# Kernel optimization log

Hardware: AMD Instinct MI355X
Metric: run time of the kernel (lower is better)

## Reference

```python
import jax, jax.numpy as jnp
import numpy as np
from jax import lax

STRIDE = 4

def grid_sample_nearest(feat, grid):
    # feat: (B, C, H, W); grid: (B, Ho, Wo, 2) normalized to [-1, 1], align_corners=True,
    # mode='nearest', padding_mode='zeros' (matches torch.nn.functional.grid_sample).
    B, C, H, W = feat.shape
    gx = (grid[..., 0] + 1.0) * 0.5 * (W - 1)
    gy = (grid[..., 1] + 1.0) * 0.5 * (H - 1)
    ix = jnp.round(gx).astype(jnp.int32)  # round-half-to-even == std::nearbyint
    iy = jnp.round(gy).astype(jnp.int32)
    valid = (ix >= 0) & (ix < W) & (iy >= 0) & (iy < H)
    ixc = jnp.clip(ix, 0, W - 1)
    iyc = jnp.clip(iy, 0, H - 1)
    out = jax.vmap(lambda f, y, x: f[:, y, x])(feat, iyc, ixc)  # (B, C, Ho, Wo)
    return out * valid[:, None, :, :].astype(feat.dtype)

def unfold_s(x, s):
    # F.unfold(x, kernel=(s,s), stride=s): (n,c,h,w) -> (n, c*s*s, h//s * w//s)
    n, c, h, w = x.shape
    h4, w4 = h // s, w // s
    x = x.reshape(n, c, h4, s, w4, s).transpose(0, 1, 3, 5, 2, 4)  # (n,c,kh,kw,h4,w4)
    return x.reshape(n, c * s * s, h4 * w4)

def fold_s(x, s, c, h, w):
    # F.fold, kernel=(s,s), stride=s (non-overlapping): (n, c*s*s, h4*w4) -> (n,c,h,w)
    n = x.shape[0]
    h4, w4 = h // s, w // s
    x = x.reshape(n, c, s, s, h4, w4).transpose(0, 1, 4, 2, 5, 3)  # (n,c,h4,kh,w4,kw)
    return x.reshape(n, c, h, w)

def _normalize(x, axis):
    return x / jnp.maximum(jnp.linalg.norm(x, axis=axis, keepdims=True), 1e-12)

def ltam_forward(curr_feat, index_feat_set_s1, anchor_feat, sparse_feat_set_s1,
                 sparse_feat_set_s2, sparse_feat_set_s3, location_feat,
                 fusion_w, fusion_b):
    s = STRIDE
    n, c, h, w = anchor_feat.shape
    t = sparse_feat_set_s1.shape[1]
    h4, w4 = h // s, w // s
    feat_len = c * s * s
    feat_num = h4 * w4

    # build normalized nearest-sampling grid from location map
    gf = location_feat.reshape(n, t, 2, h4, w4).transpose(0, 1, 3, 4, 2)  # (n,t,h4,w4,2)
    gx = 2.0 * gf[..., 0] / max(w4 - 1, 1) - 1.0
    gy = 2.0 * gf[..., 1] / max(h4 - 1, 1) - 1.0
    grid = jnp.stack([gx, gy], axis=-1).reshape(n * t, h4, w4, 2)

    def warp(fs):
        return grid_sample_nearest(fs.reshape(n * t, feat_len, h4, w4), grid)

    out_s1 = warp(sparse_feat_set_s1)   # (n*t, feat_len, h4, w4)
    out_s2 = warp(sparse_feat_set_s2)
    out_s3 = warp(sparse_feat_set_s3)
    idx_s1 = warp(index_feat_set_s1)

    # current-frame patch tokens, L2-normalized
    cf = unfold_s(curr_feat, s).transpose(0, 2, 1)          # (n, feat_num, feat_len)
    cf = _normalize(cf, axis=2)

    # index tokens per frame, L2-normalized, correlate with current tokens
    idx_tok = idx_s1.reshape(n, t, feat_len, feat_num).transpose(0, 3, 1, 2)  # (n,feat_num,t,feat_len)
    idx_tok = _normalize(idx_tok, axis=3)
    matrix_index = jnp.einsum('nptf,npf->npt', idx_tok, cf)  # (n, feat_num, t)

    corr_soft = jnp.max(matrix_index, axis=2)                # (n, feat_num)
    corr_index = jnp.argmax(matrix_index, axis=2)            # (n, feat_num)

    corr_soft_map = fold_s(jnp.broadcast_to(corr_soft[:, None, :], (n, feat_len, feat_num)),
                           s, c, h, w)                       # (n, c, h, w)

    def gather_fold(o):
        o = o.reshape(n, t, feat_len, feat_num)
        idx = jnp.broadcast_to(corr_index[:, None, None, :], (n, 1, feat_len, feat_num))
        g = jnp.take_along_axis(o, idx, axis=1)[:, 0]        # (n, feat_len, feat_num)
        return fold_s(g, s, c, h, w)

    f1 = gather_fold(out_s1)
    f2 = gather_fold(out_s2)
    f3 = gather_fold(out_s3)

    out = jnp.concatenate([f1, f2, f3], axis=1)              # (n, 3c, h, w)
    out = lax.conv_general_dilated(out, fusion_w, (1, 1), ((1, 1), (1, 1)),
                                   dimension_numbers=('NCHW', 'OIHW', 'NCHW'))
    out = out + fusion_b[None, :, None, None]
    out = out * corr_soft_map + anchor_feat
    return out

def setup_inputs() -> dict:
    key = jax.random.key(0)
    ks = jax.random.split(key, 10)
    n, t, c, h, w, s = 1, 4, 128, 192, 192, STRIDE
    h4, w4 = h // s, w // s
    feat_len = c * s * s
    inp = {
        'curr_feat': jax.random.normal(ks[0], (n, c, h, w), jnp.float32),
        'index_feat_set_s1': jax.random.normal(ks[1], (n, t, feat_len, h4, w4), jnp.float32),
        'anchor_feat': jax.random.normal(ks[2], (n, c, h, w), jnp.float32),
        'sparse_feat_set_s1': jax.random.normal(ks[3], (n, t, feat_len, h4, w4), jnp.float32),
        'sparse_feat_set_s2': jax.random.normal(ks[4], (n, t, feat_len, h4, w4), jnp.float32),
        'sparse_feat_set_s3': jax.random.normal(ks[5], (n, t, feat_len, h4, w4), jnp.float32),
        # unnormalized pixel coordinates in [0, dim-1] (h4 == w4 here)
        'location_feat': jax.random.uniform(ks[6], (n, 2 * t, h4, w4), jnp.float32) * (w4 - 1),
        'fusion_w': jax.random.normal(ks[7], (c, 3 * c, 3, 3), jnp.float32) * 0.02,
        'fusion_b': jax.random.normal(ks[8], (c,), jnp.float32) * 0.02,
    }
    return inp

def reference(curr_feat, index_feat_set_s1, anchor_feat, sparse_feat_set_s1,
              sparse_feat_set_s2, sparse_feat_set_s3, location_feat,
              fusion_w, fusion_b):
    return ltam_forward(curr_feat, index_feat_set_s1, anchor_feat, sparse_feat_set_s1,
                        sparse_feat_set_s2, sparse_feat_set_s3, location_feat,
                        fusion_w, fusion_b)
```

## Files before the change

### kernel.cpp

```cpp
#include <hip/hip_runtime.h>
#include <hip/hip_bf16.h>
#include <math.h>

#define T_FRAMES 4
#define C 128
#define H 192
#define W 192
#define H4 48
#define W4 48
#define FEAT_LEN 2048
#define FEAT_NUM 2304
#define HW (H*W)
#define NCH 384
#define KTOT 3456
#define PPX 194

typedef __bf16 bf16x8 __attribute__((ext_vector_type(8)));
typedef float f32x4 __attribute__((ext_vector_type(4)));

__device__ __forceinline__ void sample_loc(const float* __restrict__ loc, int k, int p,
                                           int& iy, int& ix, int& valid) {
    float gfx = loc[(2*k+0)*FEAT_NUM + p];
    float gfy = loc[(2*k+1)*FEAT_NUM + p];
    float gx = 2.0f*gfx/47.0f - 1.0f;
    float gy = 2.0f*gfy/47.0f - 1.0f;
    float fx = (gx + 1.0f)*0.5f*47.0f;
    float fy = (gy + 1.0f)*0.5f*47.0f;
    int jx = (int)rintf(fx);
    int jy = (int)rintf(fy);
    valid = (jx >= 0 && jx < W4 && jy >= 0 && jy < H4) ? 1 : 0;
    ix = min(max(jx, 0), W4-1);
    iy = min(max(jy, 0), H4-1);
}

__global__ __launch_bounds__(256) void k_tr(const float* __restrict__ src,
                                            float* __restrict__ dst) {
    __shared__ float lds[64*65];
    int p0 = blockIdx.x*64, f0 = blockIdx.y*64, k = blockIdx.z;
    const float* s = src + (size_t)k*FEAT_LEN*FEAT_NUM;
    float* d = dst + (size_t)k*FEAT_NUM*FEAT_LEN;
    int tid = threadIdx.x;
    int pl = tid & 63, fb = tid >> 6;
#pragma unroll
    for (int i = 0; i < 16; ++i) {
        int fl = fb*16 + i;
        lds[fl*65 + pl] = s[(size_t)(f0+fl)*FEAT_NUM + p0 + pl];
    }
    __syncthreads();
    int f4 = (tid & 15)*4, pb = tid >> 4;
#pragma unroll
    for (int i = 0; i < 4; ++i) {
        int pl2 = pb + i*16;
        float4 v = { lds[(f4+0)*65 + pl2], lds[(f4+1)*65 + pl2],
                     lds[(f4+2)*65 + pl2], lds[(f4+3)*65 + pl2] };
        *(float4*)&d[(size_t)(p0+pl2)*FEAT_LEN + f0 + f4] = v;
    }
}

__global__ __launch_bounds__(256) void k_trs(const float* __restrict__ s1,
                                             const float* __restrict__ s2,
                                             const float* __restrict__ s3,
                                             ushort* __restrict__ spT) {
    __shared__ float lds[64*65];
    int p0 = blockIdx.x*64, f0 = blockIdx.y*64;
    int z = blockIdx.z;
    int set = z >> 2, k = z & 3;
    const float* src = (set == 0) ? s1 : ((set == 1) ? s2 : s3);
    const float* s = src + (size_t)k*FEAT_LEN*FEAT_NUM;
    int tid = threadIdx.x;
    int pl = tid & 63, fb = tid >> 6;
#pragma unroll
    for (int i = 0; i < 16; ++i) {
        int fl = fb*16 + i;
        lds[fl*65 + pl] = s[(size_t)(f0+fl)*FEAT_NUM + p0 + pl];
    }
    __syncthreads();
    int fo = (tid & 7)*8, pr = tid >> 3;
#pragma unroll
    for (int i = 0; i < 2; ++i) {
        int row = pr + i*32;
        ushort vv[8];
#pragma unroll
        for (int j = 0; j < 8; ++j) {
            __hip_bfloat16 b = __float2bfloat16(lds[(fo+j)*65 + row]);
            vv[j] = *(ushort*)&b;
        }
        uint4 pk;
        pk.x = (uint)vv[0] | ((uint)vv[1] << 16);
        pk.y = (uint)vv[2] | ((uint)vv[3] << 16);
        pk.z = (uint)vv[4] | ((uint)vv[5] << 16);
        pk.w = (uint)vv[6] | ((uint)vv[7] << 16);
        *(uint4*)(spT + ((size_t)z*FEAT_NUM + p0 + row)*FEAT_LEN + f0 + fo) = pk;
    }
}

__global__ __launch_bounds__(256) void k_gather2(const ushort* __restrict__ spT,
                                                 const float* __restrict__ loc,
                                                 const int* __restrict__ corr_index,
                                                 ushort* __restrict__ cat) {
    __shared__ ushort tok[3*FEAT_LEN];
    int p = blockIdx.x;
    int y4 = p / W4, x4 = p - y4*W4;
    int tid = threadIdx.x;
    int k = corr_index[p];
    int iy, ix, valid;
    sample_loc(loc, k, p, iy, ix, valid);
    int sp = iy*W4 + ix;

#pragma unroll
    for (int j = 0; j < 3; ++j) {
        int idx = j*256 + tid;
        int set = idx >> 8, off = (idx & 255)*8;
        uint4 v = {0u,0u,0u,0u};
        if (valid)
            v = *(const uint4*)(spT + ((size_t)(set*4 + k)*FEAT_NUM + sp)*FEAT_LEN + off);
        *(uint4*)(tok + set*FEAT_LEN + off) = v;
    }
    __syncthreads();

#pragma unroll
    for (int j = 0; j < 3; ++j) {
        int idx = j*256 + tid;
        int px16 = idx / 48, oct = idx - px16*48;
        int ky = px16 >> 2, kx = px16 & 3;
        int y = y4*4 + ky, x = x4*4 + kx;
        int set = oct >> 4, c0 = (oct & 15)*8;
        int sub = (ky << 2) + kx;
        ushort vv[8];
#pragma unroll
        for (int e = 0; e < 8; ++e) vv[e] = tok[set*FEAT_LEN + ((c0 + e) << 4) + sub];
        uint4 pk;
        pk.x = (uint)vv[0] | ((uint)vv[1] << 16);
        pk.y = (uint)vv[2] | ((uint)vv[3] << 16);
        pk.z = (uint)vv[4] | ((uint)vv[5] << 16);
        pk.w = (uint)vv[6] | ((uint)vv[7] << 16);
        *(uint4*)(cat + ((size_t)(y+1)*PPX + (x+1))*NCH + set*128 + c0) = pk;
    }
}

__global__ __launch_bounds__(256) void k_corr2(const float* __restrict__ curr,
                                               const float* __restrict__ idxT,
                                               const float* __restrict__ loc,
                                               int* __restrict__ corr_index,
                                               float* __restrict__ corr_soft) {
    int p = blockIdx.x;
    int y4 = p / W4, x4 = p - y4*W4;
    int tid = threadIdx.x;

    int iy[T_FRAMES], ix[T_FRAMES], valid[T_FRAMES];
    const float* tok[T_FRAMES];
#pragma unroll
    for (int k = 0; k < T_FRAMES; ++k) {
        sample_loc(loc, k, p, iy[k], ix[k], valid[k]);
        tok[k] = idxT + ((size_t)k*FEAT_NUM + iy[k]*W4 + ix[k])*FEAT_LEN;
    }

    float ss_cf = 0.f;
    float dotk[T_FRAMES] = {0.f,0.f,0.f,0.f};
    float ssk[T_FRAMES]  = {0.f,0.f,0.f,0.f};
    int ybase = y4*4, xbase = x4*4;

#pragma unroll
    for (int it = 0; it < 2; ++it) {
        int f4 = (tid + it*256)*4;
        int cc = f4 >> 4, kh = (f4 >> 2) & 3;
        float4 cf = *(const float4*)&curr[cc*HW + (ybase+kh)*W + xbase];
        ss_cf += cf.x*cf.x + cf.y*cf.y + cf.z*cf.z + cf.w*cf.w;
#pragma unroll
        for (int k = 0; k < T_FRAMES; ++k) {
            if (valid[k]) {
                float4 v = *(const float4*)&tok[k][f4];
                dotk[k] += cf.x*v.x + cf.y*v.y + cf.z*v.z + cf.w*v.w;
                ssk[k]  += v.x*v.x + v.y*v.y + v.z*v.z + v.w*v.w;
            }
        }
    }

    float vals[9] = {ss_cf, dotk[0],dotk[1],dotk[2],dotk[3], ssk[0],ssk[1],ssk[2],ssk[3]};
#pragma unroll
    for (int j = 0; j < 9; ++j) {
        float v = vals[j];
#pragma unroll
        for (int off = 32; off > 0; off >>= 1) v += __shfl_xor(v, off, 64);
        vals[j] = v;
    }
    __shared__ float red[4][9];
    int wave = tid >> 6, lane = tid & 63;
    if (lane == 0) {
#pragma unroll
        for (int j = 0; j < 9; ++j) red[wave][j] = vals[j];
    }
    __syncthreads();
    if (tid == 0) {
        float tot[9];
#pragma unroll
        for (int j = 0; j < 9; ++j) tot[j] = red[0][j]+red[1][j]+red[2][j]+red[3][j];
        float ncf = fmaxf(sqrtf(tot[0]), 1e-12f);
        float best = -1e30f; int bestk = 0;
#pragma unroll
        for (int k = 0; k < T_FRAMES; ++k) {
            float nk = fmaxf(sqrtf(tot[5+k]), 1e-12f);
            float m = tot[1+k] / (nk * ncf);
            if (m > best) { best = m; bestk = k; }
        }
        corr_index[p] = bestk;
        corr_soft[p]  = best;
    }
}

__global__ __launch_bounds__(256) void k_corr(const float* __restrict__ curr,
                                              const float* __restrict__ idxf,
                                              const float* __restrict__ loc,
                                              int* __restrict__ corr_index,
                                              float* __restrict__ corr_soft) {
    int p = blockIdx.x;
    int y4 = p / W4, x4 = p - y4*W4;
    int tid = threadIdx.x;

    int iy[T_FRAMES], ix[T_FRAMES], valid[T_FRAMES];
#pragma unroll
    for (int k = 0; k < T_FRAMES; ++k) sample_loc(loc, k, p, iy[k], ix[k], valid[k]);

    float ss_cf = 0.f;
    float dotk[T_FRAMES] = {0.f,0.f,0.f,0.f};
    float ssk[T_FRAMES]  = {0.f,0.f,0.f,0.f};

    int ybase = y4*4, xbase = x4*4;
    for (int f = tid; f < FEAT_LEN; f += 256) {
        int cc = f >> 4;
        int kh = (f >> 2) & 3;
        int kw = f & 3;
        float cf = curr[cc*HW + (ybase+kh)*W + (xbase+kw)];
        ss_cf += cf*cf;
#pragma unroll
        for (int k = 0; k < T_FRAMES; ++k) {
            float v = 0.f;
            if (valid[k]) v = idxf[(k*FEAT_LEN + f)*FEAT_NUM + iy[k]*W4 + ix[k]];
            dotk[k] += cf*v;
            ssk[k]  += v*v;
        }
    }

    float vals[9] = {ss_cf, dotk[0],dotk[1],dotk[2],dotk[3], ssk[0],ssk[1],ssk[2],ssk[3]};
#pragma unroll
    for (int j = 0; j < 9; ++j) {
        float v = vals[j];
#pragma unroll
        for (int off = 32; off > 0; off >>= 1) v += __shfl_xor(v, off, 64);
        vals[j] = v;
    }
    __shared__ float red[4][9];
    int wave = tid >> 6, lane = tid & 63;
    if (lane == 0) {
#pragma unroll
        for (int j = 0; j < 9; ++j) red[wave][j] = vals[j];
    }
    __syncthreads();
    if (tid == 0) {
        float tot[9];
#pragma unroll
        for (int j = 0; j < 9; ++j) tot[j] = red[0][j]+red[1][j]+red[2][j]+red[3][j];
        float ncf = fmaxf(sqrtf(tot[0]), 1e-12f);
        float best = -1e30f; int bestk = 0;
#pragma unroll
        for (int k = 0; k < T_FRAMES; ++k) {
            float nk = fmaxf(sqrtf(tot[5+k]), 1e-12f);
            float m = tot[1+k] / (nk * ncf);
            if (m > best) { best = m; bestk = k; }
        }
        corr_index[p] = bestk;
        corr_soft[p]  = best;
    }
}

__global__ __launch_bounds__(256) void k_wconv(const float* __restrict__ w,
                                               ushort* __restrict__ wt) {
    int gid = blockIdx.x*256 + threadIdx.x;
    if (gid >= 128*KTOT) return;
    int o = gid / KTOT, rem = gid - o*KTOT;
    int tap = rem / NCH, i = rem - tap*NCH;
    __hip_bfloat16 b = __float2bfloat16(w[(o*NCH + i)*9 + tap]);
    wt[gid] = *(ushort*)&b;
}

__global__ __launch_bounds__(256) void k_border(ushort* __restrict__ cat) {
    int gid = blockIdx.x*256 + threadIdx.x;
    if (gid >= 772*48) return;
    int oct = gid % 48, bp = gid / 48;
    int ypad, xpad;
    if (bp < 194)      { ypad = 0;        xpad = bp; }
    else if (bp < 388) { ypad = 193;      xpad = bp - 194; }
    else if (bp < 580) { ypad = bp - 387; xpad = 0; }
    else               { ypad = bp - 579; xpad = 193; }
    uint4 z = {0u,0u,0u,0u};
    *(uint4*)(cat + (ypad*PPX + xpad)*NCH + oct*8) = z;
}

__global__ __launch_bounds__(256) void k_gather(const float* __restrict__ s1,
                                                const float* __restrict__ s2,
                                                const float* __restrict__ s3,
                                                const float* __restrict__ loc,
                                                const int* __restrict__ corr_index,
                                                ushort* __restrict__ cat) {
    int gid = blockIdx.x*256 + threadIdx.x;
    if (gid >= HW*48) return;
    int oct = gid % 48, px = gid / 48;
    int x = px % W, y = px / W;
    int p = (y >> 2)*W4 + (x >> 2);
    int k = corr_index[p];
    int iy, ix, valid;
    sample_loc(loc, k, p, iy, ix, valid);
    int set = oct >> 4;
    int c0  = (oct & 15) * 8;
    int sub = ((y & 3) << 2) + (x & 3);
    ushort v[8];
#pragma unroll
    for (int e = 0; e < 8; ++e) v[e] = 0;
    if (valid) {
        const float* src = (set == 0) ? s1 : ((set == 1) ? s2 : s3);
        const float* sp = src + (size_t)k*FEAT_LEN*FEAT_NUM + iy*W4 + ix;
#pragma unroll
        for (int e = 0; e < 8; ++e) {
            int f = ((c0 + e) << 4) + sub;
            __hip_bfloat16 b = __float2bfloat16(sp[(size_t)f*FEAT_NUM]);
            v[e] = *(ushort*)&b;
        }
    }
    uint4 pk;
    pk.x = (uint)v[0] | ((uint)v[1] << 16);
    pk.y = (uint)v[2] | ((uint)v[3] << 16);
    pk.z = (uint)v[4] | ((uint)v[5] << 16);
    pk.w = (uint)v[6] | ((uint)v[7] << 16);
    *(uint4*)(cat + ((y+1)*PPX + (x+1))*NCH + oct*8) = pk;
}

__global__ __launch_bounds__(256, 4) void k_conv2(const ushort* __restrict__ cat,
                                                  const ushort* __restrict__ wt,
                                                  const float* __restrict__ bias,
                                                  const float* __restrict__ corr_soft,
                                                  const float* __restrict__ anchor,
                                                  float* __restrict__ out) {
    __shared__ char smX[4*34*128];
    __shared__ char smW[128*128];

    int tx = blockIdx.x, ty = blockIdx.y;
    int tid = threadIdx.x;
    int wave = tid >> 6, l = tid & 63;
    int lx = l & 15, lg = l >> 4;
    int co0w = wave * 32;
    int kpart = lg * 16;

    f32x4 acc[2][4];
#pragma unroll
    for (int mf = 0; mf < 2; ++mf)
#pragma unroll
        for (int nf = 0; nf < 4; ++nf) acc[mf][nf] = (f32x4){0.f,0.f,0.f,0.f};

    int pyv[4], pxxv[4];
#pragma unroll
    for (int nf = 0; nf < 4; ++nf) { int pxl = nf*16 + lx; pyv[nf] = pxl >> 5; pxxv[nf] = pxl & 31; }
    int wbase[2], wswz[2];
#pragma unroll
    for (int mf = 0; mf < 2; ++mf) { int col = co0w + mf*16 + lx; wbase[mf] = col*128; wswz[mf] = (col & 7) << 4; }

    for (int chunk = 0; chunk < 6; ++chunk) {
        for (int idx = tid; idx < 4*34*8; idx += 256) {
            int oct = idx & 7, rc = idx >> 3;
            int r = rc / 34, xp = rc - r*34;
            const ushort* gp = cat + ((ty*2 + r)*PPX + (tx*32 + xp))*NCH + chunk*64 + oct*8;
            uint4 v = *(const uint4*)gp;
            *(uint4*)(smX + rc*128 + ((oct*16) ^ ((xp & 7) << 4))) = v;
        }
        for (int tap = 0; tap < 9; ++tap) {
#pragma unroll
            for (int q = 0; q < 4; ++q) {
                int idx = tid + q*256;
                int oct = idx & 7, col = idx >> 3;
                const ushort* gp = wt + col*KTOT + tap*NCH + chunk*64 + oct*8;
                uint4 v = *(const uint4*)gp;
                *(uint4*)(smW + col*128 + ((oct*16) ^ ((col & 7) << 4))) = v;
            }
            __syncthreads();
            int dy = tap/3 - 1, dx = tap - (tap/3)*3 - 1;
            int xrc[4], xswz[4];
#pragma unroll
            for (int nf = 0; nf < 4; ++nf) {
                int xp2 = pxxv[nf] + dx + 1;
                xrc[nf] = (pyv[nf] + dy + 1)*34 + xp2;
                xswz[nf] = (xp2 & 7) << 4;
            }
#pragma unroll
            for (int kk = 0; kk < 2; ++kk) {
                int kb = kk*64 + kpart;
                bf16x8 wf[2], xf[4];
#pragma unroll
                for (int mf = 0; mf < 2; ++mf)
                    wf[mf] = *(const bf16x8*)(smW + wbase[mf] + (kb ^ wswz[mf]));
#pragma unroll
                for (int nf = 0; nf < 4; ++nf)
                    xf[nf] = *(const bf16x8*)(smX + xrc[nf]*128 + (kb ^ xswz[nf]));
#pragma unroll
                for (int mf = 0; mf < 2; ++mf)
#pragma unroll
                    for (int nf = 0; nf < 4; ++nf)
                        acc[mf][nf] = __builtin_amdgcn_mfma_f32_16x16x32_bf16(
                            wf[mf], xf[nf], acc[mf][nf], 0, 0, 0);
            }
            __syncthreads();
        }
    }

    float cs[4]; int pixo[4];
#pragma unroll
    for (int nf = 0; nf < 4; ++nf) {
        int y = ty*2 + pyv[nf];
        int x = tx*32 + pxxv[nf];
        cs[nf] = corr_soft[(ty >> 1)*W4 + (x >> 2)];
        pixo[nf] = y*W + x;
    }
#pragma unroll
    for (int mf = 0; mf < 2; ++mf) {
#pragma unroll
        for (int j = 0; j < 4; ++j) {
            int co = co0w + mf*16 + lg*4 + j;
            float b = bias[co];
#pragma unroll
            for (int nf = 0; nf < 4; ++nf) {
                int o = co*HW + pixo[nf];
                out[o] = (acc[mf][nf][j] + b)*cs[nf] + anchor[o];
            }
        }
    }
}

extern "C" void kernel_launch(void* const* d_in, const int* in_sizes, int n_in,
                              void* d_out, int out_size, void* d_ws, size_t ws_size,
                              hipStream_t stream) {
    const float* curr   = (const float*)d_in[0];
    const float* idxf   = (const float*)d_in[1];
    const float* anchor = (const float*)d_in[2];
    const float* s1     = (const float*)d_in[3];
    const float* s2     = (const float*)d_in[4];
    const float* s3     = (const float*)d_in[5];
    const float* loc    = (const float*)d_in[6];
    const float* wgt    = (const float*)d_in[7];
    const float* bias   = (const float*)d_in[8];
    float* out = (float*)d_out;

    char* ws = (char*)d_ws;
    int*    corr_index = (int*)ws;
    float*  corr_soft  = (float*)(ws + 16384);
    ushort* wt         = (ushort*)(ws + 32768);
    ushort* cat        = (ushort*)(ws + 917504);
    char*   big        = ws + 917504 + 28912128;
    float*  idxT       = (float*)big;
    ushort* spT        = (ushort*)big;
    const size_t SPT_BYTES  = (size_t)3*T_FRAMES*FEAT_NUM*FEAT_LEN*2;
    const size_t IDXT_BYTES = (size_t)T_FRAMES*FEAT_NUM*FEAT_LEN*4;
    const size_t NEED_A = 29829632 + (SPT_BYTES > IDXT_BYTES ? SPT_BYTES : IDXT_BYTES);
    const size_t NEED_B = 917504 + IDXT_BYTES;

    if (ws_size >= NEED_A) {
        hipLaunchKernelGGL(k_tr, dim3(36, 32, 4), dim3(256), 0, stream, idxf, idxT);
        hipLaunchKernelGGL(k_corr2, dim3(FEAT_NUM), dim3(256), 0, stream,
                           curr, idxT, loc, corr_index, corr_soft);
        hipLaunchKernelGGL(k_wconv, dim3((128*KTOT + 255)/256), dim3(256), 0, stream, wgt, wt);
        hipLaunchKernelGGL(k_border, dim3((772*48 + 255)/256), dim3(256), 0, stream, cat);
        hipLaunchKernelGGL(k_trs, dim3(36, 32, 12), dim3(256), 0, stream, s1, s2, s3, spT);
        hipLaunchKernelGGL(k_gather2, dim3(FEAT_NUM), dim3(256), 0, stream,
                           spT, loc, corr_index, cat);
    } else {
        float*  idxT_b = (float*)(ws + 917504);
        ushort* cat_b  = (ushort*)(ws + 917504);
        if (ws_size >= NEED_B) {
            hipLaunchKernelGGL(k_tr, dim3(36, 32, 4), dim3(256), 0, stream, idxf, idxT_b);
            hipLaunchKernelGGL(k_corr2, dim3(FEAT_NUM), dim3(256), 0, stream,
                               curr, idxT_b, loc, corr_index, corr_soft);
        } else {
            hipLaunchKernelGGL(k_corr, dim3(FEAT_NUM), dim3(256), 0, stream,
                               curr, idxf, loc, corr_index, corr_soft);
        }
        hipLaunchKernelGGL(k_wconv, dim3((128*KTOT + 255)/256), dim3(256), 0, stream, wgt, wt);
        hipLaunchKernelGGL(k_border, dim3((772*48 + 255)/256), dim3(256), 0, stream, cat_b);
        hipLaunchKernelGGL(k_gather, dim3((HW*48 + 255)/256), dim3(256), 0, stream,
                           s1, s2, s3, loc, corr_index, cat_b);
        hipLaunchKernelGGL(k_conv2, dim3(6, 96), dim3(256), 0, stream,
                           cat_b, wt, bias, corr_soft, anchor, out);
        return;
    }
    hipLaunchKernelGGL(k_conv2, dim3(6, 96), dim3(256), 0, stream,
                       cat, wt, bias, corr_soft, anchor, out);
}
```

Baseline: 224.3 us.

## Double-buffer conv2 LDS tiles with async global_load_lds prefetch

```diff
diff --git a/kernel.cpp b/kernel.cpp
--- a/kernel.cpp
+++ b/kernel.cpp
@@ -13,10 +13,17 @@
 #define HW (H*W)
 #define NCH 384
 #define KTOT 3456
+#define NSTEP 54
 #define PPX 194
 
 typedef __bf16 bf16x8 __attribute__((ext_vector_type(8)));
 typedef float f32x4 __attribute__((ext_vector_type(4)));
+
+__device__ __forceinline__ void gl16(const void* gp, void* ldsbase) {
+    __builtin_amdgcn_global_load_lds(
+        (const __attribute__((address_space(1))) void*)gp,
+        (__attribute__((address_space(3))) void*)ldsbase, 16, 0, 0);
+}
 
 __device__ __forceinline__ void sample_loc(const float* __restrict__ loc, int k, int p,
                                            int& iy, int& ix, int& valid) {
@@ -278,8 +285,10 @@
     int gid = blockIdx.x*256 + threadIdx.x;
     if (gid >= 128*KTOT) return;
     int o = gid / KTOT, rem = gid - o*KTOT;
-    int tap = rem / NCH, i = rem - tap*NCH;
-    __hip_bfloat16 b = __float2bfloat16(w[(o*NCH + i)*9 + tap]);
+    int step = rem >> 6, ci = rem & 63;
+    int chunk = step / 9, tap = step - chunk*9;
+    int ci_g = chunk*64 + ci;
+    __hip_bfloat16 b = __float2bfloat16(w[(o*NCH + ci_g)*9 + tap]);
     wt[gid] = *(ushort*)&b;
 }
 
@@ -334,14 +343,14 @@
     *(uint4*)(cat + ((y+1)*PPX + (x+1))*NCH + oct*8) = pk;
 }
 
-__global__ __launch_bounds__(256, 4) void k_conv2(const ushort* __restrict__ cat,
+__global__ __launch_bounds__(256, 2) void k_conv2(const ushort* __restrict__ cat,
                                                   const ushort* __restrict__ wt,
                                                   const float* __restrict__ bias,
                                                   const float* __restrict__ corr_soft,
                                                   const float* __restrict__ anchor,
                                                   float* __restrict__ out) {
-    __shared__ char smX[4*34*128];
-    __shared__ char smW[128*128];
+    __shared__ char smX[2][136*128];
+    __shared__ char smW[2][128*128];
 
     int tx = blockIdx.x, ty = blockIdx.y;
     int tid = threadIdx.x;
@@ -349,6 +358,39 @@
     int lx = l & 15, lg = l >> 4;
     int co0w = wave * 32;
     int kpart = lg * 16;
+    int wbofs = (wave*64)*16;
+
+    auto stageW = [&](int step, int b) {
+#pragma unroll
+        for (int q = 0; q < 4; ++q) {
+            int idx = tid + q*256;
+            int col = idx >> 3, oct = idx & 7;
+            int octp = oct ^ (col & 7);
+            const ushort* gp = wt + ((size_t)col*NSTEP + step)*64 + octp*8;
+            gl16(gp, smW[b] + q*256*16 + wbofs);
+        }
+    };
+    auto stageX = [&](int chunk, int b) {
+#pragma unroll
+        for (int q = 0; q < 4; ++q) {
+            int idx = tid + q*256;
+            int rc = idx >> 3, oct = idx & 7;
+            int r = rc / 34, xp = rc - r*34;
+            int octp = oct ^ (xp & 7);
+            const ushort* gp = cat + ((size_t)(ty*2 + r)*PPX + (tx*32 + xp))*NCH
+                               + chunk*64 + octp*8;
+            gl16(gp, smX[b] + q*256*16 + wbofs);
+        }
+        if (wave == 0) {
+            int idx = 1024 + l;
+            int rc = idx >> 3, oct = idx & 7;
+            int xp = rc - 102;
+            int octp = oct ^ (xp & 7);
+            const ushort* gp = cat + ((size_t)(ty*2 + 3)*PPX + (tx*32 + xp))*NCH
+                               + chunk*64 + octp*8;
+            gl16(gp, smX[0] + 1024*16 + (b ? (int)sizeof(smX[0]) : 0));
+        }
+    };
 
     f32x4 acc[2][4];
 #pragma unroll
@@ -363,31 +405,26 @@
 #pragma unroll
     for (int mf = 0; mf < 2; ++mf) { int col = co0w + mf*16 + lx; wbase[mf] = col*128; wswz[mf] = (col & 7) << 4; }
 
+    stageX(0, 0);
+    stageW(0, 0);
+    __syncthreads();
+
     for (int chunk = 0; chunk < 6; ++chunk) {
-        for (int idx = tid; idx < 4*34*8; idx += 256) {
-            int oct = idx & 7, rc = idx >> 3;
-            int r = rc / 34, xp = rc - r*34;
-            const ushort* gp = cat + ((ty*2 + r)*PPX + (tx*32 + xp))*NCH + chunk*64 + oct*8;
-            uint4 v = *(const uint4*)gp;
-            *(uint4*)(smX + rc*128 + ((oct*16) ^ ((xp & 7) << 4))) = v;
-        }
+        const char* Xb = smX[chunk & 1];
+#pragma unroll
         for (int tap = 0; tap < 9; ++tap) {
-#pragma unroll
-            for (int q = 0; q < 4; ++q) {
-                int idx = tid + q*256;
-                int oct = idx & 7, col = idx >> 3;
-                const ushort* gp = wt + col*KTOT + tap*NCH + chunk*64 + oct*8;
-                uint4 v = *(const uint4*)gp;
-                *(uint4*)(smW + col*128 + ((oct*16) ^ ((col & 7) << 4))) = v;
-            }
-            __syncthreads();
-            int dy = tap/3 - 1, dx = tap - (tap/3)*3 - 1;
-            int xrc[4], xswz[4];
+            int step = chunk*9 + tap;
+            const char* Wb = smW[step & 1];
+            if (step < NSTEP-1) stageW(step+1, (step+1) & 1);
+            if (tap == 8 && chunk < 5) stageX(chunk+1, (chunk+1) & 1);
+
+            const int dy = tap/3 - 1, dx = tap%3 - 1;
+            int xrc[4], xsw[4];
 #pragma unroll
             for (int nf = 0; nf < 4; ++nf) {
                 int xp2 = pxxv[nf] + dx + 1;
                 xrc[nf] = (pyv[nf] + dy + 1)*34 + xp2;
-                xswz[nf] = (xp2 & 7) << 4;
+                xsw[nf] = (xp2 & 7) << 4;
             }
 #pragma unroll
             for (int kk = 0; kk < 2; ++kk) {
@@ -395,10 +432,10 @@
                 bf16x8 wf[2], xf[4];
 #pragma unroll
                 for (int mf = 0; mf < 2; ++mf)
-                    wf[mf] = *(const bf16x8*)(smW + wbase[mf] + (kb ^ wswz[mf]));
+                    wf[mf] = *(const bf16x8*)(Wb + wbase[mf] + (kb ^ wswz[mf]));
 #pragma unroll
                 for (int nf = 0; nf < 4; ++nf)
-                    xf[nf] = *(const bf16x8*)(smX + xrc[nf]*128 + (kb ^ xswz[nf]));
+                    xf[nf] = *(const bf16x8*)(Xb + xrc[nf]*128 + (kb ^ xsw[nf]));
 #pragma unroll
                 for (int mf = 0; mf < 2; ++mf)
 #pragma unroll
```

Result: slower. 245.6 us (+9.5%).
